# Optimization experiments

Hardware: AMD Instinct MI355X
Metric: run time of the kernel (lower is better)

Reference implementation:

```python
import jax, jax.numpy as jnp
import numpy as np

B, L, C, H, DK, MAXREL = 4, 1024, 768, 12, 64, 7
NEG = -2.0 ** 15  # masked_fill value


def _rel_pos_table(L, m):
    # abs distance, compressed logarithmically beyond m, clipped to [0, 2m]
    i = jnp.arange(L, dtype=jnp.float32)
    d = jnp.abs(i[:, None] - i[None, :])
    comp = m + jnp.log2(jnp.maximum(d - m, 1.0))
    d = jnp.where(d > m, comp, d)
    return jnp.clip(d, 0, 2 * m).astype(jnp.int32)  # [L, L]


def setup_inputs() -> dict:
    key = jax.random.key(0)
    ks = jax.random.split(key, 16)
    s = 0.02
    return {
        "qx": jax.random.normal(ks[0], (B, L, C), jnp.float32),
        "kx": jax.random.normal(ks[1], (B, L, C), jnp.float32),
        "vx": jax.random.normal(ks[2], (B, L, C), jnp.float32),
        "WQ_w": jax.random.normal(ks[3], (C, H * DK), jnp.float32) * s,
        "WQ_b": jnp.zeros((H * DK,), jnp.float32),
        "WK_w": jax.random.normal(ks[4], (C, H * DK), jnp.float32) * s,
        "WK_b": jnp.zeros((H * DK,), jnp.float32),
        "WV_w": jax.random.normal(ks[5], (C, H * DK), jnp.float32) * s,
        "WV_b": jnp.zeros((H * DK,), jnp.float32),
        "WO_w": jax.random.normal(ks[6], (H * DK, C), jnp.float32) * s,
        "WO_b": jnp.zeros((C,), jnp.float32),
        "embK": jax.random.normal(ks[7], (2 * MAXREL + 1, H), jnp.float32),
        "embB": jax.random.normal(ks[8], (2 * MAXREL + 1, H), jnp.float32) * s,
        "preScores": jax.random.normal(ks[9], (B, H, L, L), jnp.float32) * 0.1,
        "maskPAD": jnp.ones((B, L, L), jnp.int32),
    }


def reference(qx, kx, vx, WQ_w, WQ_b, WK_w, WK_b, WV_w, WV_b, WO_w, WO_b,
              embK, embB, preScores, maskPAD):
    q = (qx @ WQ_w + WQ_b).reshape(B, L, H, DK).transpose(0, 2, 1, 3)  # [B,H,L,dk]
    k = (kx @ WK_w + WK_b).reshape(B, L, H, DK).transpose(0, 2, 1, 3)
    v = (vx @ WV_w + WV_b).reshape(B, L, H, DK).transpose(0, 2, 1, 3)

    scores = jnp.einsum('bhid,bhjd->bhij', q, k) / np.sqrt(DK).astype(np.float32)

    tab = _rel_pos_table(L, MAXREL)                 # [L, L] int
    relK = jnp.transpose(embK[tab], (2, 1, 0))      # [H, L, L] (torch transpose(0,-1))
    relB = jnp.transpose(embB[tab], (2, 1, 0))
    scores = scores * relK[None] + relB[None]

    scores = scores + preScores
    scores = jnp.where((maskPAD == 0)[:, None, :, :], jnp.float32(NEG), scores)

    alpha = jax.nn.softmax(scores, axis=-1)         # dropout is identity in eval
    z = jnp.einsum('bhij,bhjd->bhid', alpha, v)     # [B,H,L,dk]
    z = z.transpose(0, 2, 1, 3).reshape(B, L, H * DK)
    z = z @ WO_w + WO_b
    return (z, scores)
```

## Files before the change

kernel.cpp:

```cpp
#include <hip/hip_runtime.h>
#include <stdint.h>


typedef __attribute__((ext_vector_type(4))) float f32x4;
typedef __attribute__((ext_vector_type(4))) int   i32x4;
typedef __attribute__((ext_vector_type(8))) short short8;
typedef __attribute__((ext_vector_type(4))) unsigned int u32x4;
typedef __attribute__((ext_vector_type(2))) unsigned int u32x2;

__device__ __forceinline__ unsigned short f2bf(float f) {
  unsigned int u = __float_as_uint(f);
  u += 0x7fffu + ((u >> 16) & 1u);
  return (unsigned short)(u >> 16);
}

__global__ __launch_bounds__(256) void conv_x_kernel(
    const float* __restrict__ qx, const float* __restrict__ kx,
    const float* __restrict__ vx, unsigned short* __restrict__ out) {
  int v = blockIdx.x * 256 + threadIdx.x;
  int mat = v / 786432;
  int r = v - mat * 786432;
  const float* src = (mat == 0) ? qx : (mat == 1) ? kx : vx;
  f32x4 x = ((const f32x4*)src)[r];
  union { unsigned short s[4]; u32x2 u; } o;
  o.s[0] = f2bf(x[0]); o.s[1] = f2bf(x[1]); o.s[2] = f2bf(x[2]); o.s[3] = f2bf(x[3]);
  ((u32x2*)out)[v] = o.u;
}

__global__ __launch_bounds__(256) void conv_mask_kernel(
    const int* __restrict__ m, unsigned int* __restrict__ out) {
  int w = blockIdx.x * 256 + threadIdx.x;
  const int* src = m + (size_t)w * 32;
  unsigned int bits = 0u;
#pragma unroll
  for (int c = 0; c < 8; c++) {
    i32x4 v = *(const i32x4*)&src[c * 4];
#pragma unroll
    for (int r = 0; r < 4; r++)
      bits |= (v[r] != 0 ? 1u : 0u) << (c * 4 + r);
  }
  out[w] = bits;
}

__global__ __launch_bounds__(256) void conv_w_kernel(
    const float* __restrict__ w0, const float* __restrict__ w1,
    const float* __restrict__ w2, const float* __restrict__ w3,
    unsigned short* __restrict__ out) {
  __shared__ float T[64][65];
  int bx = blockIdx.x;
  int mat = bx / 144; int t2 = bx - mat * 144;
  int kt = t2 / 12, nt = t2 - kt * 12;
  int k0 = kt * 64, n0 = nt * 64;
  const float* W = (mat == 0) ? w0 : (mat == 1) ? w1 : (mat == 2) ? w2 : w3;
  unsigned short* WT = out + (size_t)mat * 589824;
  int t = threadIdx.x;
  int lr = t >> 4;
  int lc = (t & 15) * 4;
#pragma unroll
  for (int p = 0; p < 4; p++) {
    int row = p * 16 + lr;
    f32x4 x = *(const f32x4*)&W[(size_t)(k0 + row) * 768 + n0 + lc];
    T[lc + 0][row] = x[0]; T[lc + 1][row] = x[1];
    T[lc + 2][row] = x[2]; T[lc + 3][row] = x[3];
  }
  __syncthreads();
#pragma unroll
  for (int p = 0; p < 4; p++) {
    int row = p * 16 + lr;
    union { unsigned short s[4]; u32x2 u; } o;
    o.s[0] = f2bf(T[row][lc + 0]); o.s[1] = f2bf(T[row][lc + 1]);
    o.s[2] = f2bf(T[row][lc + 2]); o.s[3] = f2bf(T[row][lc + 3]);
    *(u32x2*)&WT[(size_t)(n0 + row) * 768 + k0 + lc] = o.u;
  }
}

__global__ __launch_bounds__(256, 2) void qkv_gemm_kernel(
    const unsigned short* __restrict__ xbf, const unsigned short* __restrict__ wt,
    const float* __restrict__ bq, const float* __restrict__ bk, const float* __restrict__ bv,
    unsigned short* __restrict__ qo, unsigned short* __restrict__ ko,
    unsigned short* __restrict__ vto) {
  __shared__ unsigned short SM[2][2][128 * 72];
  int bx = blockIdx.x;
  int mat = bx / 192; int rem = bx - mat * 192;
  int mt = rem / 6, nt = rem - mt * 6;
  int m0 = mt * 128, n0 = nt * 128;
  const unsigned short* A = xbf + (size_t)mat * 4096 * 768;
  const unsigned short* Bm = wt + (size_t)mat * 768 * 768;
  int t = threadIdx.x;
  int wave = t >> 6, lane = t & 63;
  int wm = (wave >> 1) * 64, wn = (wave & 1) * 64;
  int col = lane & 15, quad = lane >> 4;
  int srow = t >> 3;
  int sch = (t & 7) * 8;

  f32x4 acc[4][4];
#pragma unroll
  for (int i = 0; i < 4; i++)
#pragma unroll
    for (int j = 0; j < 4; j++) acc[i][j] = (f32x4){0.f, 0.f, 0.f, 0.f};

  u32x4 ra[4], rb[4];
#pragma unroll
  for (int p = 0; p < 4; p++) {
    ra[p] = *(const u32x4*)&A[(size_t)(m0 + srow + p * 32) * 768 + sch];
    rb[p] = *(const u32x4*)&Bm[(size_t)(n0 + srow + p * 32) * 768 + sch];
  }
#pragma unroll
  for (int p = 0; p < 4; p++) {
    *(u32x4*)&SM[0][0][(srow + p * 32) * 72 + sch] = ra[p];
    *(u32x4*)&SM[0][1][(srow + p * 32) * 72 + sch] = rb[p];
  }
#pragma unroll
  for (int p = 0; p < 4; p++) {
    ra[p] = *(const u32x4*)&A[(size_t)(m0 + srow + p * 32) * 768 + 64 + sch];
    rb[p] = *(const u32x4*)&Bm[(size_t)(n0 + srow + p * 32) * 768 + 64 + sch];
  }
  __syncthreads();

  for (int it = 0; it < 12; ++it) {
    const unsigned short* As = SM[it & 1][0];
    const unsigned short* Bs = SM[it & 1][1];
#pragma unroll
    for (int c = 0; c < 2; c++) {
      short8 af[4], bf[4];
#pragma unroll
      for (int i = 0; i < 4; i++) {
        af[i] = *(const short8*)&As[(wm + i * 16 + col) * 72 + c * 32 + quad * 8];
        bf[i] = *(const short8*)&Bs[(wn + i * 16 + col) * 72 + c * 32 + quad * 8];
      }
#pragma unroll
      for (int i = 0; i < 4; i++)
#pragma unroll
        for (int j = 0; j < 4; j++)
          acc[i][j] = __builtin_amdgcn_mfma_f32_16x16x32_bf16(af[i], bf[j], acc[i][j], 0, 0, 0);
    }
    if (it < 11) {
      unsigned short* An = SM[(it + 1) & 1][0];
      unsigned short* Bn = SM[(it + 1) & 1][1];
#pragma unroll
      for (int p = 0; p < 4; p++) {
        *(u32x4*)&An[(srow + p * 32) * 72 + sch] = ra[p];
        *(u32x4*)&Bn[(srow + p * 32) * 72 + sch] = rb[p];
      }
      if (it < 10) {
        int kk2 = (it + 2) * 64;
#pragma unroll
        for (int p = 0; p < 4; p++) {
          ra[p] = *(const u32x4*)&A[(size_t)(m0 + srow + p * 32) * 768 + kk2 + sch];
          rb[p] = *(const u32x4*)&Bm[(size_t)(n0 + srow + p * 32) * 768 + kk2 + sch];
        }
      }
      __syncthreads();
    }
  }

  if (mat != 2) {
    const float* bias = (mat == 0) ? bq : bk;
    unsigned short* dst = (mat == 0) ? qo : ko;
#pragma unroll
    for (int j = 0; j < 4; j++) {
      int gn = n0 + wn + j * 16 + col;
      float bsv = bias[gn];
      int h = gn >> 6, d = gn & 63;
#pragma unroll
      for (int i = 0; i < 4; i++) {
#pragma unroll
        for (int r = 0; r < 4; r++) {
          int gm = m0 + wm + i * 16 + quad * 4 + r;
          int b = gm >> 10, l = gm & 1023;
          dst[((size_t)(b * 12 + h) * 1024 + l) * 64 + d] = f2bf(acc[i][j][r] + bsv);
        }
      }
    }
  } else {
    unsigned short* Tr = &SM[0][0][0];
    __syncthreads();
#pragma unroll
    for (int j = 0; j < 4; j++) {
      int n = wn + j * 16 + col;
      float bsv = bv[n0 + n];
#pragma unroll
      for (int i = 0; i < 4; i++) {
        int m = wm + i * 16 + quad * 4;
        union { unsigned short s[4]; u32x2 u; } pk;
#pragma unroll
        for (int r = 0; r < 4; r++) pk.s[r] = f2bf(acc[i][j][r] + bsv);
        *(u32x2*)&Tr[(size_t)n * 132 + m] = pk.u;
      }
    }
    __syncthreads();
#pragma unroll
    for (int p = 0; p < 8; p++) {
      int row = (t >> 4) + p * 16;
      int ch = (t & 15) * 8;
      u32x4 val = *(const u32x4*)&Tr[(size_t)row * 132 + ch];
      int gn = n0 + row;
      int h = gn >> 6, d = gn & 63;
      int gm = m0 + ch;
      int b = gm >> 10, l = gm & 1023;
      *(u32x4*)&vto[((size_t)(b * 12 + h) * 64 + d) * 1024 + l] = val;
    }
  }
}

struct KV { u32x4 k0, k1, v0, v1; };

__device__ __forceinline__ void attn_body(
    int jt, const unsigned short* KsC, const unsigned short* VsC,
    unsigned short* KsN, unsigned short* VsN,
    f32x4* preC, f32x4* preN, u32x2& mkC, u32x2& mkN, KV& kvW, KV& kvF,
    const short8* qf, f32x4* oacc, float& m_s, float& l_s,
    const unsigned short* kbase, const unsigned short* vbase,
    const float* pbase, const unsigned int* mrow, float* sbase,
    unsigned short* Ps, const float* eK, const float* eB,
    int lrow, int gi, int srow, int sch, int col, int quad, int wave) {
  const int j0 = jt * 64;
  if (jt < 15) {
    int jp1 = (jt + 1) * 64;
#pragma unroll
    for (int ns = 0; ns < 4; ns++)
      preN[ns] = *(const f32x4*)&pbase[(size_t)lrow * 1024 + jp1 + ns * 16 + quad * 4];
    mkN = *(const u32x2*)&mrow[(jt + 1) * 2];
  }
  if (jt < 14) {
    int jp2 = (jt + 2) * 64;
    kvF.k0 = *(const u32x4*)&kbase[(size_t)(jp2 + srow) * 64 + sch];
    kvF.k1 = *(const u32x4*)&kbase[(size_t)(jp2 + srow + 32) * 64 + sch];
    kvF.v0 = *(const u32x4*)&vbase[(size_t)srow * 1024 + jp2 + sch];
    kvF.v1 = *(const u32x4*)&vbase[(size_t)(srow + 32) * 1024 + jp2 + sch];
  }
  f32x4 sacc[4];
#pragma unroll
  for (int ns = 0; ns < 4; ns++) sacc[ns] = (f32x4){0.f, 0.f, 0.f, 0.f};
#pragma unroll
  for (int c = 0; c < 2; c++) {
#pragma unroll
    for (int ns = 0; ns < 4; ns++) {
      short8 kf = *(const short8*)&KsC[(ns * 16 + col) * 72 + c * 32 + quad * 8];
      sacc[ns] = __builtin_amdgcn_mfma_f32_16x16x32_bf16(kf, qf[c], sacc[ns], 0, 0, 0);
    }
  }
  float sv[4][4];
#pragma unroll
  for (int ns = 0; ns < 4; ns++) {
    int gj0 = j0 + ns * 16 + quad * 4;
    unsigned int hb = (mkC[ns >> 1] >> (((ns & 1) << 4) + (quad << 2))) & 0xFu;
    f32x4 sout;
#pragma unroll
    for (int r = 0; r < 4; r++) {
      int dd = gi - (gj0 + r); dd = dd < 0 ? -dd : dd;
      int idx;
      if (dd <= 7) idx = dd;
      else { idx = 38 - __clz(dd - 7); idx = idx > 14 ? 14 : idx; }
      float s = sacc[ns][r] * 0.125f * eK[idx] + eB[idx] + preC[ns][r];
      if (((hb >> r) & 1u) == 0u) s = -32768.0f;
      sout[r] = s; sv[ns][r] = s;
    }
    *(f32x4*)&sbase[(size_t)lrow * 1024 + gj0] = sout;
  }
  float mx = sv[0][0];
#pragma unroll
  for (int ns = 0; ns < 4; ns++)
#pragma unroll
    for (int r = 0; r < 4; r++) mx = fmaxf(mx, sv[ns][r]);
  mx = fmaxf(mx, __shfl_xor(mx, 16));
  mx = fmaxf(mx, __shfl_xor(mx, 32));
  float mn = fmaxf(m_s, mx);
  float alpha = __expf(m_s - mn);
  float rs = 0.f;
#pragma unroll
  for (int ns = 0; ns < 4; ns++)
#pragma unroll
    for (int r = 0; r < 4; r++) { float p = __expf(sv[ns][r] - mn); sv[ns][r] = p; rs += p; }
  rs += __shfl_xor(rs, 16); rs += __shfl_xor(rs, 32);
  l_s = l_s * alpha + rs;
  m_s = mn;
#pragma unroll
  for (int nd = 0; nd < 4; nd++)
#pragma unroll
    for (int r = 0; r < 4; r++) oacc[nd][r] *= alpha;
#pragma unroll
  for (int ns = 0; ns < 4; ns++) {
    union { unsigned short s[4]; u32x2 u; } pk;
#pragma unroll
    for (int r = 0; r < 4; r++) pk.s[r] = f2bf(sv[ns][r]);
    *(u32x2*)&Ps[(size_t)lrow * 72 + ns * 16 + quad * 4] = pk.u;
  }
#pragma unroll
  for (int c2 = 0; c2 < 2; c2++) {
    short8 pf = *(const short8*)&Ps[(wave * 16 + col) * 72 + c2 * 32 + quad * 8];
#pragma unroll
    for (int nd = 0; nd < 4; nd++) {
      short8 vf = *(const short8*)&VsC[(nd * 16 + col) * 72 + c2 * 32 + quad * 8];
      oacc[nd] = __builtin_amdgcn_mfma_f32_16x16x32_bf16(vf, pf, oacc[nd], 0, 0, 0);
    }
  }
  if (jt < 15) {
    *(u32x4*)&KsN[srow * 72 + sch] = kvW.k0;
    *(u32x4*)&KsN[(srow + 32) * 72 + sch] = kvW.k1;
    *(u32x4*)&VsN[srow * 72 + sch] = kvW.v0;
    *(u32x4*)&VsN[(srow + 32) * 72 + sch] = kvW.v1;
    __syncthreads();
  }
}

__global__ __launch_bounds__(256, 3) void attn_kernel(
    const unsigned short* __restrict__ q, const unsigned short* __restrict__ k,
    const unsigned short* __restrict__ vt, const float* __restrict__ preS,
    const unsigned int* __restrict__ maskbits, const float* __restrict__ embK,
    const float* __restrict__ embB, float* __restrict__ scores,
    unsigned short* __restrict__ zpre) {
  __shared__ unsigned short Qs[64 * 72];
  __shared__ unsigned short KsB[2][64 * 72];
  __shared__ unsigned short VsB[2][64 * 72];
  __shared__ float eKs[16], eBs[16];
  int bx = blockIdx.x;
  int slice = bx % 48, it = bx / 48;
  int b = slice / 12, h = slice - b * 12;
  int i0 = it * 64;
  int t = threadIdx.x, wave = t >> 6, lane = t & 63;
  int col = lane & 15, quad = lane >> 4;
  int srow = t >> 3, sch = (t & 7) * 8;

  if (t < 15) { eKs[t] = embK[t * 12 + h]; eBs[t] = embB[t * 12 + h]; }

  const unsigned short* qbase = q + ((size_t)(b * 12 + h) * 1024 + i0) * 64;
  const unsigned short* kbase = k + (size_t)(b * 12 + h) * 1024 * 64;
  const unsigned short* vbase = vt + (size_t)(b * 12 + h) * 64 * 1024;
  const float* pbase = preS + ((size_t)(b * 12 + h) * 1024 + i0) * 1024;
  float* sbase = scores + ((size_t)(b * 12 + h) * 1024 + i0) * 1024;
  int lrow = wave * 16 + col;
  int gi = i0 + lrow;
  const unsigned int* mrow = maskbits + ((size_t)(b * 1024 + i0 + lrow)) * 32;

#pragma unroll
  for (int p = 0; p < 2; p++) {
    int row = srow + p * 32;
    *(u32x4*)&Qs[row * 72 + sch] = *(const u32x4*)&qbase[(size_t)row * 64 + sch];
  }
  __syncthreads();
  short8 qf[2];
  qf[0] = *(const short8*)&Qs[(wave * 16 + col) * 72 + quad * 8];
  qf[1] = *(const short8*)&Qs[(wave * 16 + col) * 72 + 32 + quad * 8];

  f32x4 oacc[4];
#pragma unroll
  for (int nd = 0; nd < 4; nd++) oacc[nd] = (f32x4){0.f, 0.f, 0.f, 0.f};
  float m_s = -3.0e38f, l_s = 0.f;

  KV kvA, kvB;
  f32x4 preA[4], preB[4];
  u32x2 mkA, mkB;
  kvA.k0 = *(const u32x4*)&kbase[(size_t)srow * 64 + sch];
  kvA.k1 = *(const u32x4*)&kbase[(size_t)(srow + 32) * 64 + sch];
  kvA.v0 = *(const u32x4*)&vbase[(size_t)srow * 1024 + sch];
  kvA.v1 = *(const u32x4*)&vbase[(size_t)(srow + 32) * 1024 + sch];
  *(u32x4*)&KsB[0][srow * 72 + sch] = kvA.k0;
  *(u32x4*)&KsB[0][(srow + 32) * 72 + sch] = kvA.k1;
  *(u32x4*)&VsB[0][srow * 72 + sch] = kvA.v0;
  *(u32x4*)&VsB[0][(srow + 32) * 72 + sch] = kvA.v1;
#pragma unroll
  for (int ns = 0; ns < 4; ns++)
    preA[ns] = *(const f32x4*)&pbase[(size_t)lrow * 1024 + ns * 16 + quad * 4];
  mkA = *(const u32x2*)&mrow[0];
  kvB.k0 = *(const u32x4*)&kbase[(size_t)(64 + srow) * 64 + sch];
  kvB.k1 = *(const u32x4*)&kbase[(size_t)(64 + srow + 32) * 64 + sch];
  kvB.v0 = *(const u32x4*)&vbase[(size_t)srow * 1024 + 64 + sch];
  kvB.v1 = *(const u32x4*)&vbase[(size_t)(srow + 32) * 1024 + 64 + sch];
  __syncthreads();

  unsigned short* Ps = Qs;
  for (int n = 0; n < 16; n += 2) {
    attn_body(n,     KsB[0], VsB[0], KsB[1], VsB[1], preA, preB, mkA, mkB, kvB, kvA,
              qf, oacc, m_s, l_s, kbase, vbase, pbase, mrow, sbase,
              Ps, eKs, eBs, lrow, gi, srow, sch, col, quad, wave);
    attn_body(n + 1, KsB[1], VsB[1], KsB[0], VsB[0], preB, preA, mkB, mkA, kvA, kvB,
              qf, oacc, m_s, l_s, kbase, vbase, pbase, mrow, sbase,
              Ps, eKs, eBs, lrow, gi, srow, sch, col, quad, wave);
  }

  float inv = 1.0f / fmaxf(l_s, 1e-30f);
  unsigned short* zb = zpre + ((size_t)(b * 12 + h) * 1024 + i0 + lrow) * 64;
#pragma unroll
  for (int nd = 0; nd < 4; nd++) {
    union { unsigned short s[4]; u32x2 u; } zk;
#pragma unroll
    for (int r = 0; r < 4; r++) zk.s[r] = f2bf(oacc[nd][r] * inv);
    *(u32x2*)&zb[nd * 16 + quad * 4] = zk.u;
  }
}

__global__ __launch_bounds__(256, 3) void out_gemm_kernel(
    const unsigned short* __restrict__ zpre, const unsigned short* __restrict__ wot,
    const float* __restrict__ wob, float* __restrict__ zout) {
  __shared__ unsigned short SM[2][2][64 * 72];
  int bx = blockIdx.x;
  int mt = bx / 12, nt = bx - mt * 12;
  int m0 = mt * 64, n0 = nt * 64;
  int t = threadIdx.x;
  int wave = t >> 6, lane = t & 63;
  int wm = (wave >> 1) * 32, wn = (wave & 1) * 32;
  int col = lane & 15, quad = lane >> 4;
  int srow = t >> 3, sch = (t & 7) * 8;
  int gmA0 = m0 + srow, gmA1 = m0 + srow + 32;
  int bA0 = gmA0 >> 10, lA0 = gmA0 & 1023;
  int bA1 = gmA1 >> 10, lA1 = gmA1 & 1023;

  f32x4 acc[2][2];
#pragma unroll
  for (int i = 0; i < 2; i++)
#pragma unroll
    for (int j = 0; j < 2; j++) acc[i][j] = (f32x4){0.f, 0.f, 0.f, 0.f};

  u32x4 ra[2], rb[2];
  ra[0] = *(const u32x4*)&zpre[((size_t)(bA0 * 12 + 0) * 1024 + lA0) * 64 + sch];
  ra[1] = *(const u32x4*)&zpre[((size_t)(bA1 * 12 + 0) * 1024 + lA1) * 64 + sch];
  rb[0] = *(const u32x4*)&wot[(size_t)(n0 + srow) * 768 + sch];
  rb[1] = *(const u32x4*)&wot[(size_t)(n0 + srow + 32) * 768 + sch];
  *(u32x4*)&SM[0][0][srow * 72 + sch] = ra[0];
  *(u32x4*)&SM[0][0][(srow + 32) * 72 + sch] = ra[1];
  *(u32x4*)&SM[0][1][srow * 72 + sch] = rb[0];
  *(u32x4*)&SM[0][1][(srow + 32) * 72 + sch] = rb[1];
  ra[0] = *(const u32x4*)&zpre[((size_t)(bA0 * 12 + 1) * 1024 + lA0) * 64 + sch];
  ra[1] = *(const u32x4*)&zpre[((size_t)(bA1 * 12 + 1) * 1024 + lA1) * 64 + sch];
  rb[0] = *(const u32x4*)&wot[(size_t)(n0 + srow) * 768 + 64 + sch];
  rb[1] = *(const u32x4*)&wot[(size_t)(n0 + srow + 32) * 768 + 64 + sch];
  __syncthreads();

  for (int it = 0; it < 12; ++it) {
    const unsigned short* As = SM[it & 1][0];
    const unsigned short* Bs = SM[it & 1][1];
#pragma unroll
    for (int c = 0; c < 2; c++) {
      short8 af[2], bf[2];
#pragma unroll
      for (int i = 0; i < 2; i++) {
        af[i] = *(const short8*)&As[(wm + i * 16 + col) * 72 + c * 32 + quad * 8];
        bf[i] = *(const short8*)&Bs[(wn + i * 16 + col) * 72 + c * 32 + quad * 8];
      }
#pragma unroll
      for (int i = 0; i < 2; i++)
#pragma unroll
        for (int j = 0; j < 2; j++)
          acc[i][j] = __builtin_amdgcn_mfma_f32_16x16x32_bf16(af[i], bf[j], acc[i][j], 0, 0, 0);
    }
    if (it < 11) {
      unsigned short* An = SM[(it + 1) & 1][0];
      unsigned short* Bn = SM[(it + 1) & 1][1];
      *(u32x4*)&An[srow * 72 + sch] = ra[0];
      *(u32x4*)&An[(srow + 32) * 72 + sch] = ra[1];
      *(u32x4*)&Bn[srow * 72 + sch] = rb[0];
      *(u32x4*)&Bn[(srow + 32) * 72 + sch] = rb[1];
      if (it < 10) {
        int hh = it + 2;
        ra[0] = *(const u32x4*)&zpre[((size_t)(bA0 * 12 + hh) * 1024 + lA0) * 64 + sch];
        ra[1] = *(const u32x4*)&zpre[((size_t)(bA1 * 12 + hh) * 1024 + lA1) * 64 + sch];
        rb[0] = *(const u32x4*)&wot[(size_t)(n0 + srow) * 768 + hh * 64 + sch];
        rb[1] = *(const u32x4*)&wot[(size_t)(n0 + srow + 32) * 768 + hh * 64 + sch];
      }
      __syncthreads();
    }
  }
#pragma unroll
  for (int j = 0; j < 2; j++) {
    int gn = n0 + wn + j * 16 + col;
    float bsv = wob[gn];
#pragma unroll
    for (int i = 0; i < 2; i++) {
#pragma unroll
      for (int r = 0; r < 4; r++) {
        int gm = m0 + wm + i * 16 + quad * 4 + r;
        zout[(size_t)gm * 768 + gn] = acc[i][j][r] + bsv;
      }
    }
  }
}

extern "C" void kernel_launch(void* const* d_in, const int* in_sizes, int n_in,
                              void* d_out, int out_size, void* d_ws, size_t ws_size,
                              hipStream_t stream) {
  const float* qx   = (const float*)d_in[0];
  const float* kx   = (const float*)d_in[1];
  const float* vx   = (const float*)d_in[2];
  const float* WQ_w = (const float*)d_in[3];
  const float* WQ_b = (const float*)d_in[4];
  const float* WK_w = (const float*)d_in[5];
  const float* WK_b = (const float*)d_in[6];
  const float* WV_w = (const float*)d_in[7];
  const float* WV_b = (const float*)d_in[8];
  const float* WO_w = (const float*)d_in[9];
  const float* WO_b = (const float*)d_in[10];
  const float* embK = (const float*)d_in[11];
  const float* embB = (const float*)d_in[12];
  const float* preS = (const float*)d_in[13];
  const int* maskP  = (const int*)d_in[14];

  float* zout = (float*)d_out;
  float* scores = zout + 3145728;
  unsigned short* xbf = (unsigned short*)scores;
  unsigned int* mbits = (unsigned int*)zout;

  char* ws = (char*)d_ws;
  unsigned short* wt  = (unsigned short*)(ws);
  unsigned short* qb  = (unsigned short*)(ws + 4718592);
  unsigned short* kb  = (unsigned short*)(ws + 11010048);
  unsigned short* vtb = (unsigned short*)(ws + 17301504);
  unsigned short* zp  = (unsigned short*)(ws + 23592960);

  conv_x_kernel<<<9216, 256, 0, stream>>>(qx, kx, vx, xbf);
  conv_mask_kernel<<<512, 256, 0, stream>>>(maskP, mbits);
  conv_w_kernel<<<576, 256, 0, stream>>>(WQ_w, WK_w, WV_w, WO_w, wt);
  qkv_gemm_kernel<<<576, 256, 0, stream>>>(xbf, wt, WQ_b, WK_b, WV_b, qb, kb, vtb);
  attn_kernel<<<768, 256, 0, stream>>>(qb, kb, vtb, preS, mbits, embK, embB, scores, zp);
  out_gemm_kernel<<<192 * 4, 256, 0, stream>>>(zp, wt + 3 * 589824, WO_b, zout);
}
```

Measured before the change: 500.0 us.

## Widen attention KV tile to 128 columns with single-buffered LDS and register prefetch

The attention kernel now processes 128 key columns per iteration instead of 64. It swaps the double-buffered LDS K/V tiles for single buffers fed from register prefetch two tiles ahead. Q fragments are loaded straight from global memory rather than staged through LDS, and P gets its own shared buffer. The aim is to halve the number of loop iterations, barriers and online-softmax rescales. In exchange it uses more registers per thread (8 score accumulators, 8 preScore vectors), which may hurt occupancy under the launch bound of 3 blocks, and it adds an extra barrier per iteration.

```diff
diff --git a/kernel.cpp b/kernel.cpp
--- a/kernel.cpp
+++ b/kernel.cpp
@@ -203,116 +203,15 @@
   }
 }
 
-struct KV { u32x4 k0, k1, v0, v1; };
-
-__device__ __forceinline__ void attn_body(
-    int jt, const unsigned short* KsC, const unsigned short* VsC,
-    unsigned short* KsN, unsigned short* VsN,
-    f32x4* preC, f32x4* preN, u32x2& mkC, u32x2& mkN, KV& kvW, KV& kvF,
-    const short8* qf, f32x4* oacc, float& m_s, float& l_s,
-    const unsigned short* kbase, const unsigned short* vbase,
-    const float* pbase, const unsigned int* mrow, float* sbase,
-    unsigned short* Ps, const float* eK, const float* eB,
-    int lrow, int gi, int srow, int sch, int col, int quad, int wave) {
-  const int j0 = jt * 64;
-  if (jt < 15) {
-    int jp1 = (jt + 1) * 64;
-#pragma unroll
-    for (int ns = 0; ns < 4; ns++)
-      preN[ns] = *(const f32x4*)&pbase[(size_t)lrow * 1024 + jp1 + ns * 16 + quad * 4];
-    mkN = *(const u32x2*)&mrow[(jt + 1) * 2];
-  }
-  if (jt < 14) {
-    int jp2 = (jt + 2) * 64;
-    kvF.k0 = *(const u32x4*)&kbase[(size_t)(jp2 + srow) * 64 + sch];
-    kvF.k1 = *(const u32x4*)&kbase[(size_t)(jp2 + srow + 32) * 64 + sch];
-    kvF.v0 = *(const u32x4*)&vbase[(size_t)srow * 1024 + jp2 + sch];
-    kvF.v1 = *(const u32x4*)&vbase[(size_t)(srow + 32) * 1024 + jp2 + sch];
-  }
-  f32x4 sacc[4];
-#pragma unroll
-  for (int ns = 0; ns < 4; ns++) sacc[ns] = (f32x4){0.f, 0.f, 0.f, 0.f};
-#pragma unroll
-  for (int c = 0; c < 2; c++) {
-#pragma unroll
-    for (int ns = 0; ns < 4; ns++) {
-      short8 kf = *(const short8*)&KsC[(ns * 16 + col) * 72 + c * 32 + quad * 8];
-      sacc[ns] = __builtin_amdgcn_mfma_f32_16x16x32_bf16(kf, qf[c], sacc[ns], 0, 0, 0);
-    }
-  }
-  float sv[4][4];
-#pragma unroll
-  for (int ns = 0; ns < 4; ns++) {
-    int gj0 = j0 + ns * 16 + quad * 4;
-    unsigned int hb = (mkC[ns >> 1] >> (((ns & 1) << 4) + (quad << 2))) & 0xFu;
-    f32x4 sout;
-#pragma unroll
-    for (int r = 0; r < 4; r++) {
-      int dd = gi - (gj0 + r); dd = dd < 0 ? -dd : dd;
-      int idx;
-      if (dd <= 7) idx = dd;
-      else { idx = 38 - __clz(dd - 7); idx = idx > 14 ? 14 : idx; }
-      float s = sacc[ns][r] * 0.125f * eK[idx] + eB[idx] + preC[ns][r];
-      if (((hb >> r) & 1u) == 0u) s = -32768.0f;
-      sout[r] = s; sv[ns][r] = s;
-    }
-    *(f32x4*)&sbase[(size_t)lrow * 1024 + gj0] = sout;
-  }
-  float mx = sv[0][0];
-#pragma unroll
-  for (int ns = 0; ns < 4; ns++)
-#pragma unroll
-    for (int r = 0; r < 4; r++) mx = fmaxf(mx, sv[ns][r]);
-  mx = fmaxf(mx, __shfl_xor(mx, 16));
-  mx = fmaxf(mx, __shfl_xor(mx, 32));
-  float mn = fmaxf(m_s, mx);
-  float alpha = __expf(m_s - mn);
-  float rs = 0.f;
-#pragma unroll
-  for (int ns = 0; ns < 4; ns++)
-#pragma unroll
-    for (int r = 0; r < 4; r++) { float p = __expf(sv[ns][r] - mn); sv[ns][r] = p; rs += p; }
-  rs += __shfl_xor(rs, 16); rs += __shfl_xor(rs, 32);
-  l_s = l_s * alpha + rs;
-  m_s = mn;
-#pragma unroll
-  for (int nd = 0; nd < 4; nd++)
-#pragma unroll
-    for (int r = 0; r < 4; r++) oacc[nd][r] *= alpha;
-#pragma unroll
-  for (int ns = 0; ns < 4; ns++) {
-    union { unsigned short s[4]; u32x2 u; } pk;
-#pragma unroll
-    for (int r = 0; r < 4; r++) pk.s[r] = f2bf(sv[ns][r]);
-    *(u32x2*)&Ps[(size_t)lrow * 72 + ns * 16 + quad * 4] = pk.u;
-  }
-#pragma unroll
-  for (int c2 = 0; c2 < 2; c2++) {
-    short8 pf = *(const short8*)&Ps[(wave * 16 + col) * 72 + c2 * 32 + quad * 8];
-#pragma unroll
-    for (int nd = 0; nd < 4; nd++) {
-      short8 vf = *(const short8*)&VsC[(nd * 16 + col) * 72 + c2 * 32 + quad * 8];
-      oacc[nd] = __builtin_amdgcn_mfma_f32_16x16x32_bf16(vf, pf, oacc[nd], 0, 0, 0);
-    }
-  }
-  if (jt < 15) {
-    *(u32x4*)&KsN[srow * 72 + sch] = kvW.k0;
-    *(u32x4*)&KsN[(srow + 32) * 72 + sch] = kvW.k1;
-    *(u32x4*)&VsN[srow * 72 + sch] = kvW.v0;
-    *(u32x4*)&VsN[(srow + 32) * 72 + sch] = kvW.v1;
-    __syncthreads();
-  }
-}
-
 __global__ __launch_bounds__(256, 3) void attn_kernel(
     const unsigned short* __restrict__ q, const unsigned short* __restrict__ k,
     const unsigned short* __restrict__ vt, const float* __restrict__ preS,
     const unsigned int* __restrict__ maskbits, const float* __restrict__ embK,
     const float* __restrict__ embB, float* __restrict__ scores,
     unsigned short* __restrict__ zpre) {
-  __shared__ unsigned short Qs[64 * 72];
-  __shared__ unsigned short KsB[2][64 * 72];
-  __shared__ unsigned short VsB[2][64 * 72];
+  __shared__ unsigned short Ks[128 * 72];
+  __shared__ unsigned short Vs[64 * 136];
+  __shared__ unsigned short Ps[64 * 136];
   __shared__ float eKs[16], eBs[16];
   int bx = blockIdx.x;
   int slice = bx % 48, it = bx / 48;
@@ -320,63 +219,141 @@
   int i0 = it * 64;
   int t = threadIdx.x, wave = t >> 6, lane = t & 63;
   int col = lane & 15, quad = lane >> 4;
-  int srow = t >> 3, sch = (t & 7) * 8;
 
   if (t < 15) { eKs[t] = embK[t * 12 + h]; eBs[t] = embB[t * 12 + h]; }
 
   const unsigned short* qbase = q + ((size_t)(b * 12 + h) * 1024 + i0) * 64;
   const unsigned short* kbase = k + (size_t)(b * 12 + h) * 1024 * 64;
   const unsigned short* vbase = vt + (size_t)(b * 12 + h) * 64 * 1024;
-  const float* pbase = preS + ((size_t)(b * 12 + h) * 1024 + i0) * 1024;
-  float* sbase = scores + ((size_t)(b * 12 + h) * 1024 + i0) * 1024;
   int lrow = wave * 16 + col;
   int gi = i0 + lrow;
+  const float* prow = preS + ((size_t)(b * 12 + h) * 1024 + i0 + lrow) * 1024;
+  float* srow_p = scores + ((size_t)(b * 12 + h) * 1024 + i0 + lrow) * 1024;
   const unsigned int* mrow = maskbits + ((size_t)(b * 1024 + i0 + lrow)) * 32;
 
-#pragma unroll
-  for (int p = 0; p < 2; p++) {
-    int row = srow + p * 32;
-    *(u32x4*)&Qs[row * 72 + sch] = *(const u32x4*)&qbase[(size_t)row * 64 + sch];
-  }
-  __syncthreads();
   short8 qf[2];
-  qf[0] = *(const short8*)&Qs[(wave * 16 + col) * 72 + quad * 8];
-  qf[1] = *(const short8*)&Qs[(wave * 16 + col) * 72 + 32 + quad * 8];
+  qf[0] = *(const short8*)&qbase[(size_t)lrow * 64 + quad * 8];
+  qf[1] = *(const short8*)&qbase[(size_t)lrow * 64 + 32 + quad * 8];
+
+  int kr = t >> 3, kc = (t & 7) * 8;
+  int vr = t >> 4, vc = (t & 15) * 8;
 
   f32x4 oacc[4];
 #pragma unroll
   for (int nd = 0; nd < 4; nd++) oacc[nd] = (f32x4){0.f, 0.f, 0.f, 0.f};
   float m_s = -3.0e38f, l_s = 0.f;
 
-  KV kvA, kvB;
-  f32x4 preA[4], preB[4];
-  u32x2 mkA, mkB;
-  kvA.k0 = *(const u32x4*)&kbase[(size_t)srow * 64 + sch];
-  kvA.k1 = *(const u32x4*)&kbase[(size_t)(srow + 32) * 64 + sch];
-  kvA.v0 = *(const u32x4*)&vbase[(size_t)srow * 1024 + sch];
-  kvA.v1 = *(const u32x4*)&vbase[(size_t)(srow + 32) * 1024 + sch];
-  *(u32x4*)&KsB[0][srow * 72 + sch] = kvA.k0;
-  *(u32x4*)&KsB[0][(srow + 32) * 72 + sch] = kvA.k1;
-  *(u32x4*)&VsB[0][srow * 72 + sch] = kvA.v0;
-  *(u32x4*)&VsB[0][(srow + 32) * 72 + sch] = kvA.v1;
-#pragma unroll
-  for (int ns = 0; ns < 4; ns++)
-    preA[ns] = *(const f32x4*)&pbase[(size_t)lrow * 1024 + ns * 16 + quad * 4];
-  mkA = *(const u32x2*)&mrow[0];
-  kvB.k0 = *(const u32x4*)&kbase[(size_t)(64 + srow) * 64 + sch];
-  kvB.k1 = *(const u32x4*)&kbase[(size_t)(64 + srow + 32) * 64 + sch];
-  kvB.v0 = *(const u32x4*)&vbase[(size_t)srow * 1024 + 64 + sch];
-  kvB.v1 = *(const u32x4*)&vbase[(size_t)(srow + 32) * 1024 + 64 + sch];
+  u32x4 kvK[4], kvV[4];
+#pragma unroll
+  for (int p = 0; p < 4; p++) kvK[p] = *(const u32x4*)&kbase[(size_t)(kr + p * 32) * 64 + kc];
+#pragma unroll
+  for (int p = 0; p < 4; p++) kvV[p] = *(const u32x4*)&vbase[(size_t)(vr + p * 16) * 1024 + vc];
+#pragma unroll
+  for (int p = 0; p < 4; p++) *(u32x4*)&Ks[(kr + p * 32) * 72 + kc] = kvK[p];
+#pragma unroll
+  for (int p = 0; p < 4; p++) *(u32x4*)&Vs[(vr + p * 16) * 136 + vc] = kvV[p];
+  f32x4 preC[8];
+#pragma unroll
+  for (int ns = 0; ns < 8; ns++)
+    preC[ns] = *(const f32x4*)&prow[ns * 16 + quad * 4];
+  u32x4 mkC = *(const u32x4*)&mrow[0];
+#pragma unroll
+  for (int p = 0; p < 4; p++) kvK[p] = *(const u32x4*)&kbase[(size_t)(128 + kr + p * 32) * 64 + kc];
+#pragma unroll
+  for (int p = 0; p < 4; p++) kvV[p] = *(const u32x4*)&vbase[(size_t)(vr + p * 16) * 1024 + 128 + vc];
   __syncthreads();
 
-  unsigned short* Ps = Qs;
-  for (int n = 0; n < 16; n += 2) {
-    attn_body(n,     KsB[0], VsB[0], KsB[1], VsB[1], preA, preB, mkA, mkB, kvB, kvA,
-              qf, oacc, m_s, l_s, kbase, vbase, pbase, mrow, sbase,
-              Ps, eKs, eBs, lrow, gi, srow, sch, col, quad, wave);
-    attn_body(n + 1, KsB[1], VsB[1], KsB[0], VsB[0], preB, preA, mkB, mkA, kvA, kvB,
-              qf, oacc, m_s, l_s, kbase, vbase, pbase, mrow, sbase,
-              Ps, eKs, eBs, lrow, gi, srow, sch, col, quad, wave);
+  for (int jt = 0; jt < 8; ++jt) {
+    const int j0 = jt * 128;
+    f32x4 sacc[8];
+#pragma unroll
+    for (int ns = 0; ns < 8; ns++) sacc[ns] = (f32x4){0.f, 0.f, 0.f, 0.f};
+#pragma unroll
+    for (int c = 0; c < 2; c++) {
+#pragma unroll
+      for (int ns = 0; ns < 8; ns++) {
+        short8 kf = *(const short8*)&Ks[(ns * 16 + col) * 72 + c * 32 + quad * 8];
+        sacc[ns] = __builtin_amdgcn_mfma_f32_16x16x32_bf16(kf, qf[c], sacc[ns], 0, 0, 0);
+      }
+    }
+    float sv[8][4];
+#pragma unroll
+    for (int ns = 0; ns < 8; ns++) {
+      int gj0 = j0 + ns * 16 + quad * 4;
+      unsigned int hb = (mkC[ns >> 1] >> (((ns & 1) << 4) + (quad << 2))) & 0xFu;
+      f32x4 sout;
+#pragma unroll
+      for (int r = 0; r < 4; r++) {
+        int dd = gi - (gj0 + r); dd = dd < 0 ? -dd : dd;
+        int idx;
+        if (dd <= 7) idx = dd;
+        else { idx = 38 - __clz(dd - 7); idx = idx > 14 ? 14 : idx; }
+        float s = sacc[ns][r] * 0.125f * eKs[idx] + eBs[idx] + preC[ns][r];
+        if (((hb >> r) & 1u) == 0u) s = -32768.0f;
+        sout[r] = s; sv[ns][r] = s;
+      }
+      *(f32x4*)&srow_p[gj0] = sout;
+    }
+    float mx = sv[0][0];
+#pragma unroll
+    for (int ns = 0; ns < 8; ns++)
+#pragma unroll
+      for (int r = 0; r < 4; r++) mx = fmaxf(mx, sv[ns][r]);
+    mx = fmaxf(mx, __shfl_xor(mx, 16));
+    mx = fmaxf(mx, __shfl_xor(mx, 32));
+    float mn = fmaxf(m_s, mx);
+    float alpha = __expf(m_s - mn);
+    float rs = 0.f;
+#pragma unroll
+    for (int ns = 0; ns < 8; ns++)
+#pragma unroll
+      for (int r = 0; r < 4; r++) { float p = __expf(sv[ns][r] - mn); sv[ns][r] = p; rs += p; }
+    rs += __shfl_xor(rs, 16); rs += __shfl_xor(rs, 32);
+    l_s = l_s * alpha + rs;
+    m_s = mn;
+#pragma unroll
+    for (int nd = 0; nd < 4; nd++)
+#pragma unroll
+      for (int r = 0; r < 4; r++) oacc[nd][r] *= alpha;
+#pragma unroll
+    for (int ns = 0; ns < 8; ns++) {
+      union { unsigned short s[4]; u32x2 u; } pk;
+#pragma unroll
+      for (int r = 0; r < 4; r++) pk.s[r] = f2bf(sv[ns][r]);
+      *(u32x2*)&Ps[(size_t)lrow * 136 + ns * 16 + quad * 4] = pk.u;
+    }
+    if (jt < 7) {
+#pragma unroll
+      for (int ns = 0; ns < 8; ns++)
+        preC[ns] = *(const f32x4*)&prow[j0 + 128 + ns * 16 + quad * 4];
+      mkC = *(const u32x4*)&mrow[(jt + 1) * 4];
+    }
+#pragma unroll
+    for (int c2 = 0; c2 < 4; c2++) {
+      short8 pf = *(const short8*)&Ps[(wave * 16 + col) * 136 + c2 * 32 + quad * 8];
+#pragma unroll
+      for (int nd = 0; nd < 4; nd++) {
+        short8 vf = *(const short8*)&Vs[(nd * 16 + col) * 136 + c2 * 32 + quad * 8];
+        oacc[nd] = __builtin_amdgcn_mfma_f32_16x16x32_bf16(vf, pf, oacc[nd], 0, 0, 0);
+      }
+    }
+    __syncthreads();
+    if (jt < 7) {
+#pragma unroll
+      for (int p = 0; p < 4; p++) *(u32x4*)&Ks[(kr + p * 32) * 72 + kc] = kvK[p];
+#pragma unroll
+      for (int p = 0; p < 4; p++) *(u32x4*)&Vs[(vr + p * 16) * 136 + vc] = kvV[p];
+      if (jt < 6) {
+        int j2 = j0 + 256;
+#pragma unroll
+        for (int p = 0; p < 4; p++)
+          kvK[p] = *(const u32x4*)&kbase[(size_t)(j2 + kr + p * 32) * 64 + kc];
+#pragma unroll
+        for (int p = 0; p < 4; p++)
+          kvV[p] = *(const u32x4*)&vbase[(size_t)(vr + p * 16) * 1024 + j2 + vc];
+      }
+      __syncthreads();
+    }
   }
 
   float inv = 1.0f / fmaxf(l_s, 1e-30f);
```

Result: faster. 479.9 us (-4.0%).
